# Performance work log

Measured on AMD Instinct MI355X. Metric: run time of the kernel, lower is better.

Reference implementation:

```python
import jax, jax.numpy as jnp
import numpy as np

WS = 8        # window_size
NH = 12       # num_heads


def setup_inputs() -> dict:
    key = jax.random.key(0)
    ks = jax.random.split(key, 9)
    B, C, H, W = 4, 384, 128, 128
    s = 1.0 / np.sqrt(C)
    x = jax.random.normal(ks[0], (B, C, H, W), dtype=jnp.float32)
    Wq = jax.random.normal(ks[1], (C, C), dtype=jnp.float32) * s
    bq = jax.random.normal(ks[2], (C,), dtype=jnp.float32) * 0.01
    Wk = jax.random.normal(ks[3], (C, C), dtype=jnp.float32) * s
    bk = jax.random.normal(ks[4], (C,), dtype=jnp.float32) * 0.01
    Wv = jax.random.normal(ks[5], (C, C), dtype=jnp.float32) * s
    bv = jax.random.normal(ks[6], (C,), dtype=jnp.float32) * 0.01
    Wp = jax.random.normal(ks[7], (C, C), dtype=jnp.float32) * s
    bp = jax.random.normal(ks[8], (C,), dtype=jnp.float32) * 0.01
    return {"x": x, "Wq": Wq, "bq": bq, "Wk": Wk, "bk": bk,
            "Wv": Wv, "bv": bv, "Wp": Wp, "bp": bp}


def reference(x, Wq, bq, Wk, bk, Wv, bv, Wp, bp):
    B, C, H, W = x.shape
    ws2 = WS * WS
    dk = C // NH
    scale = dk ** -0.5

    # window_partition: flat row-major reshape (same semantics as torch's
    # reshape on a contiguous [B,C,H,W] tensor), then permute+view.
    p = x.reshape(B, H // WS, WS, W // WS, WS, C)
    p = jnp.transpose(p, (0, 5, 1, 3, 2, 4))          # [B, C, H/ws, W/ws, ws, ws]
    p = p.reshape(B, C, -1, ws2)                       # [B, C, nW, ws*ws]

    def conv1x1(w, b):  # 1x1 Conv2d on [B,C,nW,ws2]
        return jnp.einsum('bcnw,oc->bonw', p, w) + b[None, :, None, None]

    def heads(t):  # permute(0,2,3,1).contiguous().reshape -> [B, NH, nW, ws2, dk]
        t = jnp.transpose(t, (0, 2, 3, 1))             # [B, nW, ws2, C]
        return t.reshape(B, NH, -1, ws2, dk)           # row-major reinterpretation

    q = heads(conv1x1(Wq, bq))
    k = heads(conv1x1(Wk, bk))
    v = heads(conv1x1(Wv, bv))

    scores = jnp.einsum('bhnqd,bhnkd->bhnqk', q, k) * scale
    attn = jax.nn.softmax(scores, axis=-1)
    o = jnp.einsum('bhnqk,bhnkd->bhnqd', attn, v)      # [B, NH, nW, ws2, dk]
    o = o.reshape(B, -1, ws2, C)                       # [B, nW, ws2, C]

    # window_unpartition
    u = o.reshape(B, -1, WS, WS, C)
    u = jnp.transpose(u, (0, 4, 1, 2, 3))              # [B, C, nW, ws, ws]
    u = u.reshape(B, C, H, W)

    y = jnp.einsum('bchw,oc->bohw', u, Wp) + bp[None, :, None, None]
    return y
```

## Files before the change

### kernel.cpp

```cpp
#include <hip/hip_runtime.h>
#include <hip/hip_bf16.h>
#include <stdint.h>


typedef __bf16 bf16_t;
typedef __bf16 bf16x8 __attribute__((ext_vector_type(8)));
typedef __bf16 bf16x4 __attribute__((ext_vector_type(4)));
typedef float f32x4 __attribute__((ext_vector_type(4)));

__device__ __forceinline__ void gload_lds16(const void* g, void* l) {
  __builtin_amdgcn_global_load_lds((__attribute__((address_space(1))) void*)(g),
                                   (__attribute__((address_space(3))) void*)(l),
                                   16, 0, 0);
}

__global__ __launch_bounds__(256) void convw_kernel(
    const float* __restrict__ wq, const float* __restrict__ wk,
    const float* __restrict__ wv, const float* __restrict__ wp,
    bf16_t* __restrict__ oq, bf16_t* __restrict__ ok,
    bf16_t* __restrict__ ov, bf16_t* __restrict__ op_) {
  int i = blockIdx.x * 256 + threadIdx.x;
  oq[i] = (bf16_t)wq[i];
  ok[i] = (bf16_t)wk[i];
  ov[i] = (bf16_t)wv[i];
  op_[i] = (bf16_t)wp[i];
}

__global__ __launch_bounds__(256) void prep_kernel(const float* __restrict__ x,
                                                   bf16_t* __restrict__ Xp) {
  int gid = blockIdx.x * 256 + threadIdx.x;
  int row = gid / 96;
  int c4 = (gid - row * 96) * 4;
  int b = row >> 14;
  int pp = row & 16383;
  int n1 = pp >> 10, n3 = (pp >> 6) & 15, w2 = (pp >> 3) & 7, w4 = pp & 7;
  int P = (n1 << 10) | (w2 << 7) | (n3 << 3) | w4;
  float4 v = *(const float4*)(x + (size_t)((b << 14) | P) * 384 + c4);
  bf16x4 o;
  o[0] = (bf16_t)v.x; o[1] = (bf16_t)v.y; o[2] = (bf16_t)v.z; o[3] = (bf16_t)v.w;
  *(bf16x4*)(Xp + (size_t)row * 384 + c4) = o;
}

__device__ __forceinline__ void gemm_mainloop(const bf16_t* __restrict__ Arows,
                                              const bf16_t* __restrict__ Brows,
                                              bf16_t* As, bf16_t* Bs,
                                              int tid, f32x4 acc[4][4]) {
  const int lane = tid & 63, wv = tid >> 6;
  const int l15 = lane & 15, hi = lane >> 4;
  const int wr = wv >> 1, wc = wv & 1;
  for (int kt = 0; kt < 12; ++kt) {
    const int k0 = kt * 32;
#pragma unroll
    for (int j = 0; j < 2; ++j) {
      int q = wv * 128 + j * 64 + lane;
      int row = q >> 2, c16 = q & 3;
      gload_lds16(Arows + (size_t)row * 384 + k0 + c16 * 8,
                  (char*)As + (wv * 128 + j * 64) * 16);
      gload_lds16(Brows + (size_t)row * 384 + k0 + c16 * 8,
                  (char*)Bs + (wv * 128 + j * 64) * 16);
    }
    __syncthreads();
    bf16x8 a[4], b[4];
#pragma unroll
    for (int i = 0; i < 4; ++i) {
      a[i] = *(const bf16x8*)(As + (wr * 64 + i * 16 + l15) * 32 + hi * 8);
      b[i] = *(const bf16x8*)(Bs + (wc * 64 + i * 16 + l15) * 32 + hi * 8);
    }
#pragma unroll
    for (int mi = 0; mi < 4; ++mi)
#pragma unroll
      for (int ni = 0; ni < 4; ++ni)
        acc[mi][ni] = __builtin_amdgcn_mfma_f32_16x16x32_bf16(a[mi], b[ni],
                                                              acc[mi][ni], 0, 0, 0);
    __syncthreads();
  }
}

__global__ __launch_bounds__(256) void qkv_gemm(
    const bf16_t* __restrict__ Xp,
    const bf16_t* __restrict__ Wqb, const bf16_t* __restrict__ Wkb,
    const bf16_t* __restrict__ Wvb,
    const float* __restrict__ bq, const float* __restrict__ bk,
    const float* __restrict__ bv,
    bf16_t* __restrict__ Qs, bf16_t* __restrict__ Ks, bf16_t* __restrict__ Vs) {
  __shared__ __align__(16) bf16_t As[128 * 32];
  __shared__ __align__(16) bf16_t Bs[128 * 32];
  const int tid = threadIdx.x;
  const int m0 = blockIdx.x * 128;
  const int n0 = blockIdx.y * 128;
  const int which = blockIdx.z;
  const bf16_t* W = which == 0 ? Wqb : (which == 1 ? Wkb : Wvb);
  const float* bias = which == 0 ? bq : (which == 1 ? bk : bv);
  bf16_t* Out = which == 0 ? Qs : (which == 1 ? Ks : Vs);
  f32x4 acc[4][4] = {};
  gemm_mainloop(Xp + (size_t)m0 * 384, W + (size_t)n0 * 384, As, Bs, tid, acc);
  const int lane = tid & 63, wv = tid >> 6;
  const int l15 = lane & 15, hi = lane >> 4;
  const int wr = wv >> 1, wc = wv & 1;
#pragma unroll
  for (int ni = 0; ni < 4; ++ni) {
    int chan = n0 + wc * 64 + ni * 16 + l15;
    float bv_ = bias[chan];
#pragma unroll
    for (int mi = 0; mi < 4; ++mi)
#pragma unroll
      for (int r = 0; r < 4; ++r) {
        int row = m0 + wr * 64 + mi * 16 + hi * 4 + r;
        Out[(size_t)row * 384 + chan] = (bf16_t)(acc[mi][ni][r] + bv_);
      }
  }
}

__global__ __launch_bounds__(64) void attn_kernel(const bf16_t* __restrict__ Q,
                                                  const bf16_t* __restrict__ K,
                                                  const bf16_t* __restrict__ V,
                                                  bf16_t* __restrict__ O) {
  const size_t base = (size_t)blockIdx.x * 2048;
  const bf16_t* q = Q + base;
  const bf16_t* k = K + base;
  const bf16_t* v = V + base;
  bf16_t* o = O + base;
  const int lane = threadIdx.x;
  const int l15 = lane & 15, hi = lane >> 4;

  __shared__ __align__(16) bf16_t Vt[32][72];
  __shared__ __align__(16) bf16_t Ps[64][72];

#pragma unroll
  for (int j = 0; j < 4; ++j) {
    bf16x8 vv = *(const bf16x8*)(v + lane * 32 + j * 8);
#pragma unroll
    for (int e = 0; e < 8; ++e) Vt[j * 8 + e][lane] = vv[e];
  }

  bf16x8 aQ[4], bK[4];
#pragma unroll
  for (int i = 0; i < 4; ++i) {
    aQ[i] = *(const bf16x8*)(q + (i * 16 + l15) * 32 + hi * 8);
    bK[i] = *(const bf16x8*)(k + (i * 16 + l15) * 32 + hi * 8);
  }
  f32x4 sc[4][4] = {};
#pragma unroll
  for (int mi = 0; mi < 4; ++mi)
#pragma unroll
    for (int ni = 0; ni < 4; ++ni)
      sc[mi][ni] = __builtin_amdgcn_mfma_f32_16x16x32_bf16(aQ[mi], bK[ni],
                                                           sc[mi][ni], 0, 0, 0);

  const float SCALE = 0.17677669529663687f;
  float rs[4][4];
#pragma unroll
  for (int mi = 0; mi < 4; ++mi) {
#pragma unroll
    for (int r = 0; r < 4; ++r) {
      float s0 = sc[mi][0][r] * SCALE, s1 = sc[mi][1][r] * SCALE;
      float s2 = sc[mi][2][r] * SCALE, s3 = sc[mi][3][r] * SCALE;
      float mx = fmaxf(fmaxf(s0, s1), fmaxf(s2, s3));
      mx = fmaxf(mx, __shfl_xor(mx, 1));
      mx = fmaxf(mx, __shfl_xor(mx, 2));
      mx = fmaxf(mx, __shfl_xor(mx, 4));
      mx = fmaxf(mx, __shfl_xor(mx, 8));
      float p0 = __expf(s0 - mx), p1 = __expf(s1 - mx);
      float p2 = __expf(s2 - mx), p3 = __expf(s3 - mx);
      int row = mi * 16 + hi * 4 + r;
      Ps[row][0 + l15] = (bf16_t)p0;
      Ps[row][16 + l15] = (bf16_t)p1;
      Ps[row][32 + l15] = (bf16_t)p2;
      Ps[row][48 + l15] = (bf16_t)p3;
      float sum = p0 + p1 + p2 + p3;
      sum += __shfl_xor(sum, 1);
      sum += __shfl_xor(sum, 2);
      sum += __shfl_xor(sum, 4);
      sum += __shfl_xor(sum, 8);
      rs[mi][r] = sum;
    }
  }
  __syncthreads();

  f32x4 oacc[4][2] = {};
#pragma unroll
  for (int mi = 0; mi < 4; ++mi)
#pragma unroll
    for (int ks = 0; ks < 2; ++ks) {
      bf16x8 aP = *(const bf16x8*)(&Ps[mi * 16 + l15][ks * 32 + hi * 8]);
#pragma unroll
      for (int n2 = 0; n2 < 2; ++n2) {
        bf16x8 bV = *(const bf16x8*)(&Vt[n2 * 16 + l15][ks * 32 + hi * 8]);
        oacc[mi][n2] = __builtin_amdgcn_mfma_f32_16x16x32_bf16(aP, bV,
                                                               oacc[mi][n2], 0, 0, 0);
      }
    }
#pragma unroll
  for (int mi = 0; mi < 4; ++mi)
#pragma unroll
    for (int n2 = 0; n2 < 2; ++n2)
#pragma unroll
      for (int r = 0; r < 4; ++r) {
        int row = mi * 16 + hi * 4 + r;
        o[row * 32 + n2 * 16 + l15] = (bf16_t)(oacc[mi][n2][r] / rs[mi][r]);
      }
}

__global__ __launch_bounds__(256) void proj_gemm(const bf16_t* __restrict__ Wpb,
                                                 const bf16_t* __restrict__ O,
                                                 const float* __restrict__ bp,
                                                 float* __restrict__ y) {
  __shared__ __align__(16) bf16_t As[128 * 32];
  __shared__ __align__(16) bf16_t Bs[128 * 32];
  const int tid = threadIdx.x;
  const int n0 = blockIdx.x * 128;
  const int m0 = blockIdx.y * 128;
  const int b = blockIdx.z;
  f32x4 acc[4][4] = {};
  gemm_mainloop(Wpb + (size_t)m0 * 384, O + ((size_t)b * 16384 + n0) * 384,
                As, Bs, tid, acc);
  const int lane = tid & 63, wv = tid >> 6;
  const int l15 = lane & 15, hi = lane >> 4;
  const int wr = wv >> 1, wc = wv & 1;
  float* yb = y + (size_t)b * 6291456;
#pragma unroll
  for (int mi = 0; mi < 4; ++mi)
#pragma unroll
    for (int r = 0; r < 4; ++r) {
      int och = m0 + wr * 64 + mi * 16 + hi * 4 + r;
      float bpv = bp[och];
#pragma unroll
      for (int ni = 0; ni < 4; ++ni) {
        int pix = n0 + wc * 64 + ni * 16 + l15;
        yb[(size_t)och * 16384 + pix] = acc[mi][ni][r] + bpv;
      }
    }
}

extern "C" void kernel_launch(void* const* d_in, const int* in_sizes, int n_in,
                              void* d_out, int out_size, void* d_ws, size_t ws_size,
                              hipStream_t stream) {
  const float* x  = (const float*)d_in[0];
  const float* Wq = (const float*)d_in[1];
  const float* bq = (const float*)d_in[2];
  const float* Wk = (const float*)d_in[3];
  const float* bk = (const float*)d_in[4];
  const float* Wv = (const float*)d_in[5];
  const float* bv = (const float*)d_in[6];
  const float* Wp = (const float*)d_in[7];
  const float* bp = (const float*)d_in[8];
  float* y = (float*)d_out;

  char* ws = (char*)d_ws;
  const size_t SZ = 50331648;
  bf16_t* Xp  = (bf16_t*)(ws);
  bf16_t* Vs  = (bf16_t*)(ws + SZ);
  bf16_t* Wqb = (bf16_t*)(ws + 2 * SZ);
  bf16_t* Wkb = Wqb + 147456;
  bf16_t* Wvb = Wkb + 147456;
  bf16_t* Wpb = Wvb + 147456;
  bf16_t* Qs  = (bf16_t*)d_out;
  bf16_t* Ks  = (bf16_t*)((char*)d_out + SZ);
  bf16_t* Ob  = Xp;

  convw_kernel<<<576, 256, 0, stream>>>(Wq, Wk, Wv, Wp, Wqb, Wkb, Wvb, Wpb);
  prep_kernel<<<24576, 256, 0, stream>>>(x, Xp);
  qkv_gemm<<<dim3(512, 3, 3), 256, 0, stream>>>(Xp, Wqb, Wkb, Wvb, bq, bk, bv,
                                                Qs, Ks, Vs);
  attn_kernel<<<12288, 64, 0, stream>>>(Qs, Ks, Vs, Ob);
  proj_gemm<<<dim3(128, 3, 4), 256, 0, stream>>>(Wpb, Ob, bp, y);
}
```

Baseline: 212.0 us.

## Double-buffer GEMM LDS tiles and remap blocks for XCD-local reuse

The shared GEMM mainloop now double-buffers its LDS tiles. It prefetches k-tile kt+2 while computing kt, using explicit vmcnt waits and raw barriers instead of __syncthreads before and after every tile. Both GEMMs switch to a 1D grid whose block index is decoded so that consecutive blocks on the same XCD share the same activation row tile across the weight column tiles, which should improve L2 reuse. LDS use doubles per block, and correctness now depends on the hand-written waitcnt counts matching the outstanding async loads.

Result: faster. 194.3 us (-8.4%).

```diff
diff --git a/kernel.cpp b/kernel.cpp
--- a/kernel.cpp
+++ b/kernel.cpp
@@ -41,30 +41,42 @@
   *(bf16x4*)(Xp + (size_t)row * 384 + c4) = o;
 }
 
+__device__ __forceinline__ void stage_tile(const bf16_t* __restrict__ A,
+                                           const bf16_t* __restrict__ B,
+                                           bf16_t* As, bf16_t* Bs, int k0, int tid) {
+  const int lane = tid & 63, wv = tid >> 6;
+#pragma unroll
+  for (int j = 0; j < 2; ++j) {
+    int q = wv * 128 + j * 64 + lane;
+    int row = q >> 2, c16 = q & 3;
+    gload_lds16(A + (size_t)row * 384 + k0 + c16 * 8,
+                (char*)As + (wv * 128 + j * 64) * 16);
+    gload_lds16(B + (size_t)row * 384 + k0 + c16 * 8,
+                (char*)Bs + (wv * 128 + j * 64) * 16);
+  }
+}
+
 __device__ __forceinline__ void gemm_mainloop(const bf16_t* __restrict__ Arows,
                                               const bf16_t* __restrict__ Brows,
                                               bf16_t* As, bf16_t* Bs,
                                               int tid, f32x4 acc[4][4]) {
-  const int lane = tid & 63, wv = tid >> 6;
-  const int l15 = lane & 15, hi = lane >> 4;
-  const int wr = wv >> 1, wc = wv & 1;
+  const int lane = tid & 63;
+  const int l15 = lane & 15, hi = lane >> 4;
+  const int wr = (tid >> 6) >> 1, wc = (tid >> 6) & 1;
+  stage_tile(Arows, Brows, As, Bs, 0, tid);
+  stage_tile(Arows, Brows, As + 4096, Bs + 4096, 32, tid);
+#pragma unroll
   for (int kt = 0; kt < 12; ++kt) {
-    const int k0 = kt * 32;
-#pragma unroll
-    for (int j = 0; j < 2; ++j) {
-      int q = wv * 128 + j * 64 + lane;
-      int row = q >> 2, c16 = q & 3;
-      gload_lds16(Arows + (size_t)row * 384 + k0 + c16 * 8,
-                  (char*)As + (wv * 128 + j * 64) * 16);
-      gload_lds16(Brows + (size_t)row * 384 + k0 + c16 * 8,
-                  (char*)Bs + (wv * 128 + j * 64) * 16);
-    }
-    __syncthreads();
+    bf16_t* Ab = As + (kt & 1) * 4096;
+    bf16_t* Bb = Bs + (kt & 1) * 4096;
+    if (kt == 11) asm volatile("s_waitcnt vmcnt(0)" ::: "memory");
+    else          asm volatile("s_waitcnt vmcnt(4)" ::: "memory");
+    __builtin_amdgcn_s_barrier();
     bf16x8 a[4], b[4];
 #pragma unroll
     for (int i = 0; i < 4; ++i) {
-      a[i] = *(const bf16x8*)(As + (wr * 64 + i * 16 + l15) * 32 + hi * 8);
-      b[i] = *(const bf16x8*)(Bs + (wc * 64 + i * 16 + l15) * 32 + hi * 8);
+      a[i] = *(const bf16x8*)(Ab + (wr * 64 + i * 16 + l15) * 32 + hi * 8);
+      b[i] = *(const bf16x8*)(Bb + (wc * 64 + i * 16 + l15) * 32 + hi * 8);
     }
 #pragma unroll
     for (int mi = 0; mi < 4; ++mi)
@@ -72,34 +84,41 @@
       for (int ni = 0; ni < 4; ++ni)
         acc[mi][ni] = __builtin_amdgcn_mfma_f32_16x16x32_bf16(a[mi], b[ni],
                                                               acc[mi][ni], 0, 0, 0);
-    __syncthreads();
+    asm volatile("s_waitcnt lgkmcnt(0)" ::: "memory");
+    __builtin_amdgcn_sched_barrier(0);
+    __builtin_amdgcn_s_barrier();
+    if (kt + 2 < 12)
+      stage_tile(Arows, Brows, Ab, Bb, (kt + 2) * 32, tid);
   }
 }
 
 __global__ __launch_bounds__(256) void qkv_gemm(
-    const bf16_t* __restrict__ Xp,
-    const bf16_t* __restrict__ Wqb, const bf16_t* __restrict__ Wkb,
-    const bf16_t* __restrict__ Wvb,
+    const bf16_t* __restrict__ Xp, const bf16_t* __restrict__ Wcat,
     const float* __restrict__ bq, const float* __restrict__ bk,
     const float* __restrict__ bv,
     bf16_t* __restrict__ Qs, bf16_t* __restrict__ Ks, bf16_t* __restrict__ Vs) {
-  __shared__ __align__(16) bf16_t As[128 * 32];
-  __shared__ __align__(16) bf16_t Bs[128 * 32];
+  __shared__ __align__(16) bf16_t As[2 * 128 * 32];
+  __shared__ __align__(16) bf16_t Bs[2 * 128 * 32];
   const int tid = threadIdx.x;
-  const int m0 = blockIdx.x * 128;
-  const int n0 = blockIdx.y * 128;
-  const int which = blockIdx.z;
-  const bf16_t* W = which == 0 ? Wqb : (which == 1 ? Wkb : Wvb);
+  const int F = blockIdx.x;
+  const int xcd = F & 7;
+  const int t = F >> 3;
+  const int j = t % 9;
+  const int gq = t / 9;
+  const int m0 = (gq * 8 + xcd) * 128;
+  const int which = j / 3;
+  const int cb = (j % 3) * 128;
   const float* bias = which == 0 ? bq : (which == 1 ? bk : bv);
   bf16_t* Out = which == 0 ? Qs : (which == 1 ? Ks : Vs);
   f32x4 acc[4][4] = {};
-  gemm_mainloop(Xp + (size_t)m0 * 384, W + (size_t)n0 * 384, As, Bs, tid, acc);
+  gemm_mainloop(Xp + (size_t)m0 * 384, Wcat + (size_t)j * 128 * 384,
+                As, Bs, tid, acc);
   const int lane = tid & 63, wv = tid >> 6;
   const int l15 = lane & 15, hi = lane >> 4;
   const int wr = wv >> 1, wc = wv & 1;
 #pragma unroll
   for (int ni = 0; ni < 4; ++ni) {
-    int chan = n0 + wc * 64 + ni * 16 + l15;
+    int chan = cb + wc * 64 + ni * 16 + l15;
     float bv_ = bias[chan];
 #pragma unroll
     for (int mi = 0; mi < 4; ++mi)
@@ -205,12 +224,18 @@
                                                  const bf16_t* __restrict__ O,
                                                  const float* __restrict__ bp,
                                                  float* __restrict__ y) {
-  __shared__ __align__(16) bf16_t As[128 * 32];
-  __shared__ __align__(16) bf16_t Bs[128 * 32];
+  __shared__ __align__(16) bf16_t As[2 * 128 * 32];
+  __shared__ __align__(16) bf16_t Bs[2 * 128 * 32];
   const int tid = threadIdx.x;
-  const int n0 = blockIdx.x * 128;
-  const int m0 = blockIdx.y * 128;
-  const int b = blockIdx.z;
+  const int F = blockIdx.x;
+  const int xcd = F & 7;
+  const int t = F >> 3;
+  const int j = t % 3;
+  const int gq = t / 3;
+  const int g = gq * 8 + xcd;
+  const int n0 = (g & 127) * 128;
+  const int b = g >> 7;
+  const int m0 = j * 128;
   f32x4 acc[4][4] = {};
   gemm_mainloop(Wpb + (size_t)m0 * 384, O + ((size_t)b * 16384 + n0) * 384,
                 As, Bs, tid, acc);
@@ -250,18 +275,17 @@
   const size_t SZ = 50331648;
   bf16_t* Xp  = (bf16_t*)(ws);
   bf16_t* Vs  = (bf16_t*)(ws + SZ);
-  bf16_t* Wqb = (bf16_t*)(ws + 2 * SZ);
-  bf16_t* Wkb = Wqb + 147456;
+  bf16_t* Wcat = (bf16_t*)(ws + 2 * SZ);
+  bf16_t* Wkb = Wcat + 147456;
   bf16_t* Wvb = Wkb + 147456;
   bf16_t* Wpb = Wvb + 147456;
   bf16_t* Qs  = (bf16_t*)d_out;
   bf16_t* Ks  = (bf16_t*)((char*)d_out + SZ);
   bf16_t* Ob  = Xp;
 
-  convw_kernel<<<576, 256, 0, stream>>>(Wq, Wk, Wv, Wp, Wqb, Wkb, Wvb, Wpb);
+  convw_kernel<<<576, 256, 0, stream>>>(Wq, Wk, Wv, Wp, Wcat, Wkb, Wvb, Wpb);
   prep_kernel<<<24576, 256, 0, stream>>>(x, Xp);
-  qkv_gemm<<<dim3(512, 3, 3), 256, 0, stream>>>(Xp, Wqb, Wkb, Wvb, bq, bk, bv,
-                                                Qs, Ks, Vs);
+  qkv_gemm<<<4608, 256, 0, stream>>>(Xp, Wcat, bq, bk, bv, Qs, Ks, Vs);
   attn_kernel<<<12288, 64, 0, stream>>>(Qs, Ks, Vs, Ob);
-  proj_gemm<<<dim3(128, 3, 4), 256, 0, stream>>>(Wpb, Ob, bp, y);
-}
+  proj_gemm<<<1536, 256, 0, stream>>>(Wpb, Ob, bp, y);
+}
```
